# Kernel optimization log

Measured on AMD Instinct MI355X. Metric: run time of the kernel, lower is better.

Reference implementation:

```python
import jax, jax.numpy as jnp
import numpy as np

SEQ, MEM, B, H, NH, HD = 1024, 1024, 4, 1024, 16, 64
TOT = SEQ + MEM
RLEN = TOT
SCALE = 1.0 / np.sqrt(HD).astype(np.float32)
LN_EPS = 1e-5


def setup_inputs() -> dict:
    key = jax.random.key(0)
    ks = jax.random.split(key, 10)
    w = 0.02  # weight init scale
    # causal mask over memory+current segment: query i may attend keys j <= i + MEM
    i = jnp.arange(SEQ)[:, None]
    j = jnp.arange(TOT)[None, :]
    mask2d = j > (i + MEM)  # [SEQ, TOT] bool
    attn_mask = jnp.broadcast_to(mask2d[:, :, None], (SEQ, TOT, B))
    return {
        "x": jax.random.normal(ks[0], (SEQ, B, H), jnp.float32),
        "pos_embed": jax.random.normal(ks[1], (RLEN, H), jnp.float32),
        "r_w_bias": jax.random.normal(ks[2], (NH, HD), jnp.float32) * w,
        "r_r_bias": jax.random.normal(ks[3], (NH, HD), jnp.float32) * w,
        "attn_mask": attn_mask,
        "memory": jax.random.normal(ks[4], (MEM, B, H), jnp.float32),
        "W_qkv": jax.random.normal(ks[5], (3 * NH * HD, H), jnp.float32) * w,
        "W_r": jax.random.normal(ks[6], (NH * HD, H), jnp.float32) * w,
        "W_o": jax.random.normal(ks[7], (H, NH * HD), jnp.float32) * w,
        "ln_w": jnp.ones((H,), jnp.float32),
        "ln_b": jnp.zeros((H,), jnp.float32),
    }


def _layer_norm(x, w, b):
    mu = jnp.mean(x, axis=-1, keepdims=True)
    var = jnp.mean(jnp.square(x - mu), axis=-1, keepdims=True)
    return (x - mu) * jax.lax.rsqrt(var + LN_EPS) * w + b


def _rel_shift(x):
    # x: [i, j, b, n]; TXL rel-shift via pad-reshape-drop trick
    i, j, b, n = x.shape
    zp = jnp.zeros((i, 1, b, n), x.dtype)
    xp = jnp.concatenate([zp, x], axis=1)          # [i, j+1, b, n]
    xp = xp.reshape(j + 1, i, b, n)                # reinterpret row-major layout
    return xp[1:].reshape(i, j, b, n)


def reference(x, pos_embed, r_w_bias, r_r_bias, attn_mask, memory, W_qkv, W_r, W_o, ln_w, ln_b):
    full = jnp.concatenate([memory, x], axis=0)    # [TOT, B, H]
    w_heads = full @ W_qkv.T                       # [TOT, B, 3*NH*HD]
    q, k, v = jnp.split(w_heads, 3, axis=-1)
    q = q[-SEQ:].reshape(SEQ, B, NH, HD)
    k = k.reshape(TOT, B, NH, HD)
    v = v.reshape(TOT, B, NH, HD)
    r_k = (pos_embed @ W_r.T).reshape(RLEN, NH, HD)

    attn_ac = jnp.einsum('ibnd,jbnd->ijbn', q + r_w_bias, k)   # content score
    attn_bd = jnp.einsum('ibnd,jnd->ijbn', q + r_r_bias, r_k)  # position score
    attn_bd = _rel_shift(attn_bd)
    score = (attn_ac + attn_bd) * SCALE            # [SEQ, TOT, B, NH]
    score = jnp.where(attn_mask[:, :, :, None], -jnp.inf, score)
    prob = jax.nn.softmax(score, axis=1)           # softmax over key dim
    # dropout layers are identity in eval mode
    attn_vec = jnp.einsum('ijbn,jbnd->ibnd', prob, v).reshape(SEQ, B, NH * HD)
    attn_out = attn_vec @ W_o.T                    # [SEQ, B, H]
    return _layer_norm(x + attn_out, ln_w, ln_b)   # post-LN (pre_lnorm=False)
```

## Files before the change

### kernel.cpp

```cpp
#include <hip/hip_runtime.h>
#include <stdint.h>

typedef unsigned short u16;
typedef __bf16 bf16t;
typedef bf16t bf16x8 __attribute__((ext_vector_type(8)));
typedef float f32x4 __attribute__((ext_vector_type(4)));

#define DEV static __device__ __forceinline__

DEV u16 f2b(float f) {
  unsigned u = __float_as_uint(f);
  return (u16)((u + 0x7fffu + ((u >> 16) & 1u)) >> 16);
}
DEV u16 bcast(float f) {
  union { bf16t b; u16 u; } c;
  c.b = (bf16t)f;
  return c.u;
}
DEV float b2f(u16 h) { return __uint_as_float(((unsigned)h) << 16); }
DEV f32x4 fzero() { f32x4 v = {0.f, 0.f, 0.f, 0.f}; return v; }
DEV f32x4 mfma16(bf16x8 a, bf16x8 b, f32x4 c) {
  return __builtin_amdgcn_mfma_f32_16x16x32_bf16(a, b, c, 0, 0, 0);
}
DEV float exp2fast(float x) { return __builtin_amdgcn_exp2f(x); }

#define SEQ 1024
#define MEML 1024
#define BB 4
#define HH 1024
#define NHH 16
#define HDD 64
#define TOT 2048


__global__ __launch_bounds__(256) void k_pack(const float* __restrict__ mem,
                                              const float* __restrict__ x,
                                              u16* __restrict__ full) {
  size_t id4 = (size_t)blockIdx.x * 256 + threadIdx.x;
  size_t base = id4 * 4;
  int t = (int)(base >> 12);
  int rem = (int)(base & 4095);
  const float* src = (t < MEML) ? (mem + ((size_t)t << 12) + rem)
                                : (x + ((size_t)(t - MEML) << 12) + rem);
  float4 v = *(const float4*)src;
  ushort4 o;
  o.x = f2b(v.x); o.y = f2b(v.y); o.z = f2b(v.z); o.w = f2b(v.w);
  *(ushort4*)(full + base) = o;
}

__global__ __launch_bounds__(256) void k_cvt(const float* __restrict__ src,
                                             u16* __restrict__ dst, int n4) {
  int id = blockIdx.x * 256 + threadIdx.x;
  if (id >= n4) return;
  size_t base = (size_t)id * 4;
  float4 v = *(const float4*)(src + base);
  ushort4 o;
  o.x = f2b(v.x); o.y = f2b(v.y); o.z = f2b(v.z); o.w = f2b(v.w);
  *(ushort4*)(dst + base) = o;
}


template <int BM, int BN, int MF, int NF>
DEV void gemm_core(const u16* __restrict__ A, int lda, const u16* __restrict__ Bt,
                   int ldb, int K, f32x4 (&acc)[MF][NF]) {
  constexpr int WM = 16 * MF, WN = 16 * NF;
  constexpr int WAVES_M = BM / WM, WAVES_N = BN / WN;
  constexpr int THREADS = WAVES_M * WAVES_N * 64;
  constexpr int ITA = (BM * 4) / THREADS;
  constexpr int ITB = (BN * 4) / THREADS;
  __shared__ u16 As[BM * 40];
  __shared__ u16 Bs[BN * 40];
  const int tid = threadIdx.x, lane = tid & 63, wave = tid >> 6;
  const int wm = wave / WAVES_N, wn = wave % WAVES_N;
#pragma unroll
  for (int fm = 0; fm < MF; ++fm)
#pragma unroll
    for (int fn = 0; fn < NF; ++fn) acc[fm][fn] = fzero();

  for (int k0 = 0; k0 < K; k0 += 32) {
    __syncthreads();
#pragma unroll
    for (int it = 0; it < ITA; ++it) {
      int c = tid + it * THREADS;
      int r = c >> 2, kc = c & 3;
      *(uint4*)(As + r * 40 + kc * 8) =
          *(const uint4*)(A + (size_t)r * lda + k0 + kc * 8);
    }
#pragma unroll
    for (int it = 0; it < ITB; ++it) {
      int c = tid + it * THREADS;
      int r = c >> 2, kc = c & 3;
      *(uint4*)(Bs + r * 40 + kc * 8) =
          *(const uint4*)(Bt + (size_t)r * ldb + k0 + kc * 8);
    }
    __syncthreads();
    bf16x8 af[MF], bfr[NF];
#pragma unroll
    for (int fm = 0; fm < MF; ++fm)
      af[fm] = *(const bf16x8*)(As + (wm * WM + fm * 16 + (lane & 15)) * 40 +
                                ((lane >> 4) << 3));
#pragma unroll
    for (int fn = 0; fn < NF; ++fn)
      bfr[fn] = *(const bf16x8*)(Bs + (wn * WN + fn * 16 + (lane & 15)) * 40 +
                                 ((lane >> 4) << 3));
#pragma unroll
    for (int fm = 0; fm < MF; ++fm)
#pragma unroll
      for (int fn = 0; fn < NF; ++fn)
        acc[fm][fn] = mfma16(af[fm], bfr[fn], acc[fm][fn]);
  }
}

template <int BM, int BN, int MF, int NF, class F>
DEV void epi_apply(f32x4 (&acc)[MF][NF], F&& f) {
  constexpr int WAVES_N = BN / (16 * NF);
  const int lane = threadIdx.x & 63, wave = threadIdx.x >> 6;
  const int wm = wave / WAVES_N, wn = wave % WAVES_N;
#pragma unroll
  for (int fm = 0; fm < MF; ++fm)
#pragma unroll
    for (int fn = 0; fn < NF; ++fn)
#pragma unroll
      for (int q = 0; q < 4; ++q) {
        int rl = wm * (16 * MF) + fm * 16 + ((lane >> 4) << 2) + q;
        int cl = wn * (16 * NF) + fn * 16 + (lane & 15);
        f(rl, cl, acc[fm][fn][q]);
      }
}


__global__ __launch_bounds__(256) void k_gemm_qkv(
    const u16* __restrict__ full, const u16* __restrict__ wqkv,
    const float* __restrict__ rwb, const float* __restrict__ rrb,
    u16* __restrict__ qw, u16* __restrict__ qr, u16* __restrict__ kk,
    u16* __restrict__ vt) {
  f32x4 acc[4][4];
  const u16* A = full + (size_t)blockIdx.x * 128 * 1024;
  const u16* Bt = wqkv + (size_t)blockIdx.y * 128 * 1024;
  gemm_core<128, 128, 4, 4>(A, 1024, Bt, 1024, 1024, acc);
  const int row0 = blockIdx.x * 128, col0 = blockIdx.y * 128;
  epi_apply<128, 128, 4, 4>(acc, [&](int rl, int cl, float v) {
    int grow = row0 + rl, gcol = col0 + cl;
    int t = grow >> 2, bb = grow & 3;
    int which = gcol >> 10, hd = gcol & 1023;
    int n = hd >> 6, d = hd & 63;
    if (which == 0) {
      if (t >= MEML) {
        int i = t - MEML;
        size_t o = ((size_t)(bb * NHH + n) * SEQ + i) * HDD + d;
        qw[o] = f2b(v + rwb[hd]);
        qr[o] = f2b(v + rrb[hd]);
      }
    } else if (which == 1) {
      kk[((size_t)(bb * NHH + n) * TOT + t) * HDD + d] = f2b(v);
    } else {
      vt[((size_t)(bb * NHH + n) * HDD + d) * TOT + t] = f2b(v);
    }
  });
}

__global__ __launch_bounds__(256) void k_gemm_rk(const u16* __restrict__ pos,
                                                 const u16* __restrict__ wr,
                                                 u16* __restrict__ rk) {
  f32x4 acc[4][4];
  const u16* A = pos + (size_t)blockIdx.x * 128 * 1024;
  const u16* Bt = wr + (size_t)blockIdx.y * 128 * 1024;
  gemm_core<128, 128, 4, 4>(A, 1024, Bt, 1024, 1024, acc);
  const int row0 = blockIdx.x * 128, col0 = blockIdx.y * 128;
  epi_apply<128, 128, 4, 4>(acc, [&](int rl, int cl, float v) {
    int r = row0 + rl, o = col0 + cl;
    int n = o >> 6, d = o & 63;
    rk[((size_t)n * TOT + r) * HDD + d] = f2b(v);
  });
}

__global__ __launch_bounds__(256) void k_gemm_out(const u16* __restrict__ avec,
                                                  const u16* __restrict__ wo,
                                                  const float* __restrict__ x,
                                                  float* __restrict__ y) {
  f32x4 acc[4][4];
  const u16* A = avec + (size_t)blockIdx.x * 128 * 1024;
  const u16* Bt = wo + (size_t)blockIdx.y * 128 * 1024;
  gemm_core<128, 128, 4, 4>(A, 1024, Bt, 1024, 1024, acc);
  const int row0 = blockIdx.x * 128, col0 = blockIdx.y * 128;
  epi_apply<128, 128, 4, 4>(acc, [&](int rl, int cl, float v) {
    size_t o = (size_t)(row0 + rl) * HH + (col0 + cl);
    y[o] = v + x[o];
  });
}


__global__ __launch_bounds__(256, 2) void k_flash(
    const u16* __restrict__ qw, const u16* __restrict__ qr,
    const u16* __restrict__ kk, const u16* __restrict__ rk,
    const u16* __restrict__ vt, u16* __restrict__ avec) {
  __shared__ __align__(16) u16 Kb[2 * 4096];
  __shared__ __align__(16) u16 Vb[2 * 4096];
  __shared__ __align__(16) u16 BDp[64 * 136];
  __shared__ __align__(16) u16 Ps[4 * 1024];
  const int tid = threadIdx.x, lane = tid & 63, w = tid >> 6;
  const int l15 = lane & 15, g = lane >> 4;
  const int bid = blockIdx.x;
  const int work = (bid & 7) * 128 + (bid >> 3);
  const int ti = work & 15, pair = work >> 4;
  const int n = pair & 15, b = pair >> 4;
  const int i0 = ti * 64;
  const int bn = b * NHH + n;
  const u16* qwb = qw + ((size_t)bn * SEQ + i0) * HDD;
  const u16* qrb = qr + ((size_t)bn * SEQ + i0) * HDD;
  const u16* kbase = kk + (size_t)bn * TOT * HDD;
  const u16* rbase = rk + (size_t)n * TOT * HDD;
  const u16* vbase = vt + (size_t)bn * HDD * TOT;

  bf16x8 qwf[2], qrf[2];
#pragma unroll
  for (int ks = 0; ks < 2; ++ks) {
    int off = (w * 16 + l15) * HDD + ks * 32 + (g << 3);
    qwf[ks] = *(const bf16x8*)(qwb + off);
    qrf[ks] = *(const bf16x8*)(qrb + off);
  }

  const float NEGINF = -__builtin_inff();
  const float C2 = 0.125f * 1.44269504089f;
  f32x4 oacc[4];
#pragma unroll
  for (int db = 0; db < 4; ++db) oacc[db] = fzero();
  float mrow[4] = {NEGINF, NEGINF, NEGINF, NEGINF};
  float lrow[4] = {0.f, 0.f, 0.f, 0.f};

  const int m0 = 15 - ti;
  const int jtc = ti + 17;

  const int sr = (w << 4) + (lane >> 3);
  const int sc = (lane & 7) << 3;

  int bd_rd[16], bd_rs[16];
#pragma unroll
  for (int fn = 0; fn < 4; ++fn)
#pragma unroll
    for (int q = 0; q < 4; ++q) {
      int di = (w << 4) + (g << 2) + q;
      int dj = (fn << 4) + l15;
      int rl = (63 + dj - di) & 63;
      int s0 = ((1023 - i0 + dj - di) >> 6) & 1;
      int a0 = rl * 136 + s0 * 68 + di;
      int a1 = rl * 136 + (s0 ^ 1) * 68 + di;
      bd_rd[fn * 4 + q] = a0;
      bd_rs[fn * 4 + q] = a0 + a1;
    }
  int bd_wr[4], bd_ws[4];
  {
    int colw = (w << 4) + (g << 2);
    int sA = m0 & 1;
#pragma unroll
    for (int fn = 0; fn < 4; ++fn) {
      int wl = (fn << 4) + l15;
      int a0 = wl * 136 + sA * 68 + colw;
      int a1 = wl * 136 + (sA ^ 1) * 68 + colw;
      bd_wr[fn] = a0;
      bd_ws[fn] = a0 + a1;
    }
  }
  int ps_wr[16];
#pragma unroll
  for (int fn = 0; fn < 4; ++fn)
#pragma unroll
    for (int q = 0; q < 4; ++q) {
      int row = (g << 2) + q;
      ps_wr[fn * 4 + q] =
          (w << 10) + (row << 6) + ((((fn << 4) + l15)) ^ ((row & 7) << 3));
    }
  const int psr0 = (w << 10) + (l15 << 6) + ((g << 3) ^ ((l15 & 7) << 3));
  const int psr1 = psr0 ^ 32;
  int kr0 = (l15 << 6) + ((g << 3) ^ ((l15 & 7) << 3));
  int kr1 = kr0 ^ 32;
  int vr0 = kr0, vr1 = kr1;
  const int kwb = (sr << 6) + (sc ^ ((sr & 7) << 3));

  int koff = (64 + sr) * 64 + sc;
  int voff0 = sr * 2048 + 64 + sc;
  int voff1 = voff0 + 8 * 2048;
  int rvo[4];
#pragma unroll
  for (int fn = 0; fn < 4; ++fn)
    rvo[fn] = (((m0 + 2) << 6) + (fn << 4) + l15) * 64 + (g << 3);

  uint4 kg0, kg1, vg0, vg1;
  bf16x8 rfr[8];

  auto bd_comp_store = [&]() {
    f32x4 bd[4];
#pragma unroll
    for (int fn = 0; fn < 4; ++fn) bd[fn] = fzero();
#pragma unroll
    for (int ks = 0; ks < 2; ++ks)
#pragma unroll
      for (int fn = 0; fn < 4; ++fn)
        bd[fn] = mfma16(qrf[ks], rfr[ks * 4 + fn], bd[fn]);
#pragma unroll
    for (int fn = 0; fn < 4; ++fn) {
      ushort4 pk = {bcast(bd[fn][0] * C2), bcast(bd[fn][1] * C2),
                    bcast(bd[fn][2] * C2), bcast(bd[fn][3] * C2)};
      *(ushort4*)(BDp + bd_wr[fn]) = pk;
      bd_wr[fn] = bd_ws[fn] - bd_wr[fn];
    }
  };

  kg0 = *(const uint4*)(kbase + sr * 64 + sc);
  kg1 = *(const uint4*)(kbase + (sr + 8) * 64 + sc);
  vg0 = *(const uint4*)(vbase + sr * 2048 + sc);
  vg1 = *(const uint4*)(vbase + (sr + 8) * 2048 + sc);
#pragma unroll
  for (int fn = 0; fn < 4; ++fn) {
    int ro = ((m0 << 6) + (fn << 4) + l15) * 64 + (g << 3);
#pragma unroll
    for (int ks = 0; ks < 2; ++ks)
      rfr[ks * 4 + fn] = *(const bf16x8*)(rbase + ro + ks * 32);
  }
  bd_comp_store();
#pragma unroll
  for (int fn = 0; fn < 4; ++fn) {
    int ro = (((m0 + 1) << 6) + (fn << 4) + l15) * 64 + (g << 3);
#pragma unroll
    for (int ks = 0; ks < 2; ++ks)
      rfr[ks * 4 + fn] = *(const bf16x8*)(rbase + ro + ks * 32);
  }
  bd_comp_store();
  *(uint4*)(Kb + kwb) = kg0;
  *(uint4*)(Kb + kwb + 512) = kg1;
  *(uint4*)(Vb + kwb) = vg0;
  *(uint4*)(Vb + kwb + 512) = vg1;
  __syncthreads();
  int kw = kwb ^ 4096;

  for (int jt = 0; jt < jtc; ++jt) {
    const bool haveStage = (jt + 1 < jtc);
    const bool haveBD = (jt + 3 <= jtc);
    if (haveStage) {
      kg0 = *(const uint4*)(kbase + koff);
      kg1 = *(const uint4*)(kbase + koff + 512);
      vg0 = *(const uint4*)(vbase + voff0);
      vg1 = *(const uint4*)(vbase + voff1);
    }
    if (haveBD) {
#pragma unroll
      for (int fn = 0; fn < 4; ++fn)
#pragma unroll
        for (int ks = 0; ks < 2; ++ks)
          rfr[ks * 4 + fn] = *(const bf16x8*)(rbase + rvo[fn] + ks * 32);
    }

    f32x4 ac[4];
#pragma unroll
    for (int fn = 0; fn < 4; ++fn) ac[fn] = fzero();
#pragma unroll
    for (int fn = 0; fn < 4; ++fn) {
      bf16x8 kf = *(const bf16x8*)(Kb + kr0 + fn * 1024);
      ac[fn] = mfma16(qwf[0], kf, ac[fn]);
    }
#pragma unroll
    for (int fn = 0; fn < 4; ++fn) {
      bf16x8 kf = *(const bf16x8*)(Kb + kr1 + fn * 1024);
      ac[fn] = mfma16(qwf[1], kf, ac[fn]);
    }

    const bool last = (jt == jtc - 1);
    float pmax[4] = {NEGINF, NEGINF, NEGINF, NEGINF};
#pragma unroll
    for (int fn = 0; fn < 4; ++fn)
#pragma unroll
      for (int q = 0; q < 4; ++q) {
        float bdv = b2f(BDp[bd_rd[fn * 4 + q]]);
        float sv = __builtin_fmaf(ac[fn][q], C2, bdv);
        if (last) {
          int di = (g << 2) + q;
          int dj = (fn << 4) + l15 - (w << 4);
          if (dj > di) sv = NEGINF;
        }
        ac[fn][q] = sv;
        pmax[q] = fmaxf(pmax[q], sv);
      }
#pragma unroll
    for (int q = 0; q < 4; ++q) {
#pragma unroll
      for (int off = 1; off < 16; off <<= 1)
        pmax[q] = fmaxf(pmax[q], __shfl_xor(pmax[q], off, 64));
    }
    int need = (pmax[0] > mrow[0] + 8.f) | (pmax[1] > mrow[1] + 8.f) |
               (pmax[2] > mrow[2] + 8.f) | (pmax[3] > mrow[3] + 8.f);
    if (__any(need)) {
#pragma unroll
      for (int q = 0; q < 4; ++q) {
        float mn = fmaxf(mrow[q], pmax[q]);
        float sc2 = exp2fast(mrow[q] - mn);
        mrow[q] = mn;
        lrow[q] *= sc2;
#pragma unroll
        for (int db = 0; db < 4; ++db) oacc[db][q] *= sc2;
      }
    }
#pragma unroll
    for (int fn = 0; fn < 4; ++fn)
#pragma unroll
      for (int q = 0; q < 4; ++q) {
        float p = exp2fast(ac[fn][q] - mrow[q]);
        lrow[q] += p;
        Ps[ps_wr[fn * 4 + q]] = bcast(p);
      }
    {
      bf16x8 pa0 = *(const bf16x8*)(Ps + psr0);
      bf16x8 pa1 = *(const bf16x8*)(Ps + psr1);
#pragma unroll
      for (int db = 0; db < 4; ++db) {
        bf16x8 vf = *(const bf16x8*)(Vb + vr0 + db * 1024);
        oacc[db] = mfma16(pa0, vf, oacc[db]);
      }
#pragma unroll
      for (int db = 0; db < 4; ++db) {
        bf16x8 vf = *(const bf16x8*)(Vb + vr1 + db * 1024);
        oacc[db] = mfma16(pa1, vf, oacc[db]);
      }
    }
    if (haveBD) bd_comp_store();
    if (haveStage) {
      *(uint4*)(Kb + kw) = kg0;
      *(uint4*)(Kb + kw + 512) = kg1;
      *(uint4*)(Vb + kw) = vg0;
      *(uint4*)(Vb + kw + 512) = vg1;
    }
    __syncthreads();
#pragma unroll
    for (int e = 0; e < 16; ++e) bd_rd[e] = bd_rs[e] - bd_rd[e];
    kr0 ^= 4096; kr1 ^= 4096; vr0 ^= 4096; vr1 ^= 4096; kw ^= 4096;
    koff += 4096; voff0 += 64; voff1 += 64;
#pragma unroll
    for (int fn = 0; fn < 4; ++fn) rvo[fn] += 4096;
  }

#pragma unroll
  for (int q = 0; q < 4; ++q) {
#pragma unroll
    for (int off = 1; off < 16; off <<= 1)
      lrow[q] += __shfl_xor(lrow[q], off, 64);
    lrow[q] = 1.f / lrow[q];
  }
#pragma unroll
  for (int db = 0; db < 4; ++db)
#pragma unroll
    for (int q = 0; q < 4; ++q) {
      int i = i0 + (w << 4) + (g << 2) + q;
      avec[((size_t)i * BB + b) * HH + n * HDD + db * 16 + l15] =
          bcast(oacc[db][q] * lrow[q]);
    }
}


__global__ __launch_bounds__(256) void k_ln(const float* __restrict__ y,
                                            const float* __restrict__ lw,
                                            const float* __restrict__ lb,
                                            float* __restrict__ out) {
  const int row = blockIdx.x, tid = threadIdx.x;
  const float4 v = *(const float4*)(y + (size_t)row * HH + tid * 4);
  float s = v.x + v.y + v.z + v.w;
  float ss = v.x * v.x + v.y * v.y + v.z * v.z + v.w * v.w;
#pragma unroll
  for (int off = 1; off < 64; off <<= 1) {
    s += __shfl_xor(s, off, 64);
    ss += __shfl_xor(ss, off, 64);
  }
  __shared__ float red[8];
  const int w = tid >> 6, lane = tid & 63;
  if (lane == 0) { red[w] = s; red[4 + w] = ss; }
  __syncthreads();
  float tot = red[0] + red[1] + red[2] + red[3];
  float tss = red[4] + red[5] + red[6] + red[7];
  float mu = tot * (1.f / 1024.f);
  float var = tss * (1.f / 1024.f) - mu * mu;
  float rs = rsqrtf(var + 1e-5f);
  float4 wv = *(const float4*)(lw + tid * 4);
  float4 bv = *(const float4*)(lb + tid * 4);
  float4 o;
  o.x = (v.x - mu) * rs * wv.x + bv.x;
  o.y = (v.y - mu) * rs * wv.y + bv.y;
  o.z = (v.z - mu) * rs * wv.z + bv.z;
  o.w = (v.w - mu) * rs * wv.w + bv.w;
  *(float4*)(out + (size_t)row * HH + tid * 4) = o;
}


extern "C" void kernel_launch(void* const* d_in, const int* in_sizes, int n_in,
                              void* d_out, int out_size, void* d_ws,
                              size_t ws_size, hipStream_t stream) {
  const float* x = (const float*)d_in[0];
  const float* pos = (const float*)d_in[1];
  const float* rwb = (const float*)d_in[2];
  const float* rrb = (const float*)d_in[3];
  const float* mem = (const float*)d_in[5];
  const float* wqkv = (const float*)d_in[6];
  const float* wr = (const float*)d_in[7];
  const float* wo = (const float*)d_in[8];
  const float* lnw = (const float*)d_in[9];
  const float* lnb = (const float*)d_in[10];

  char* ws = (char*)d_ws;
  const size_t O_FULL = 0;
  const size_t O_WQKV = 16777216;
  const size_t O_WR = 23068672;
  const size_t O_WO = 25165824;
  const size_t O_POS = 27262976;
  const size_t O_QW = 31457280;
  const size_t O_QR = 39845888;
  const size_t O_K = 48234496;
  const size_t O_VT = 65011712;
  const size_t O_RK = 81788928;
  const size_t O_AVEC = 85983232;
  const size_t NEED = 94371840;

  if (ws_size < NEED) return;

  u16* full = (u16*)(ws + O_FULL);
  u16* wqkv_b = (u16*)(ws + O_WQKV);
  u16* wr_b = (u16*)(ws + O_WR);
  u16* wo_b = (u16*)(ws + O_WO);
  u16* pos_b = (u16*)(ws + O_POS);
  u16* qw = (u16*)(ws + O_QW);
  u16* qr = (u16*)(ws + O_QR);
  u16* kk = (u16*)(ws + O_K);
  u16* vt = (u16*)(ws + O_VT);
  u16* rk = (u16*)(ws + O_RK);
  u16* avec = (u16*)(ws + O_AVEC);
  float* y = (float*)(ws + O_FULL);

  k_pack<<<8192, 256, 0, stream>>>(mem, x, full);
  k_cvt<<<3072, 256, 0, stream>>>(wqkv, wqkv_b, 786432);
  k_cvt<<<1024, 256, 0, stream>>>(wr, wr_b, 262144);
  k_cvt<<<1024, 256, 0, stream>>>(wo, wo_b, 262144);
  k_cvt<<<2048, 256, 0, stream>>>(pos, pos_b, 524288);

  k_gemm_qkv<<<dim3(64, 24), 256, 0, stream>>>(full, wqkv_b, rwb, rrb, qw, qr,
                                               kk, vt);
  k_gemm_rk<<<dim3(16, 8), 256, 0, stream>>>(pos_b, wr_b, rk);

  k_flash<<<dim3(1024), 256, 0, stream>>>(qw, qr, kk, rk, vt, avec);

  k_gemm_out<<<dim3(32, 8), 256, 0, stream>>>(avec, wo_b, x, y);
  k_ln<<<4096, 256, 0, stream>>>(y, lnw, lnb, (float*)d_out);
}
```

Baseline: 340.6 us.

## Load GEMM tiles directly into LDS and schedule heavy attention tiles first

The shared GEMM core now copies A and B tiles from global memory straight into LDS with 16-byte global_load_lds, instead of staging them through registers. The LDS tiles become unpadded with a 32-element row stride so each wave's lane-ordered writes land contiguously. That unpadded layout can cause more LDS bank conflicts on the fragment reads. Separately, the flash attention kernel reverses the query-tile order so the tiles with the most unmasked keys are scheduled first, which should improve load balance across CUs.

```diff
diff --git a/kernel.cpp b/kernel.cpp
--- a/kernel.cpp
+++ b/kernel.cpp
@@ -23,6 +23,11 @@
   return __builtin_amdgcn_mfma_f32_16x16x32_bf16(a, b, c, 0, 0, 0);
 }
 DEV float exp2fast(float x) { return __builtin_amdgcn_exp2f(x); }
+DEV void gload16(const u16* g, u16* l) {
+  __builtin_amdgcn_global_load_lds(
+      (const __attribute__((address_space(1))) unsigned int*)g,
+      (__attribute__((address_space(3))) unsigned int*)l, 16, 0, 0);
+}
 
 #define SEQ 1024
 #define MEML 1024
@@ -60,49 +65,42 @@
 }
 
 
-template <int BM, int BN, int MF, int NF>
-DEV void gemm_core(const u16* __restrict__ A, int lda, const u16* __restrict__ Bt,
-                   int ldb, int K, f32x4 (&acc)[MF][NF]) {
-  constexpr int WM = 16 * MF, WN = 16 * NF;
-  constexpr int WAVES_M = BM / WM, WAVES_N = BN / WN;
-  constexpr int THREADS = WAVES_M * WAVES_N * 64;
-  constexpr int ITA = (BM * 4) / THREADS;
-  constexpr int ITB = (BN * 4) / THREADS;
-  __shared__ u16 As[BM * 40];
-  __shared__ u16 Bs[BN * 40];
+template <int MF, int NF>
+DEV void gemm_core2(const u16* __restrict__ A, int lda,
+                    const u16* __restrict__ Bt, int ldb, int K,
+                    f32x4 (&acc)[MF][NF]) {
+  __shared__ __align__(16) u16 As[128 * 32];
+  __shared__ __align__(16) u16 Bs[128 * 32];
   const int tid = threadIdx.x, lane = tid & 63, wave = tid >> 6;
-  const int wm = wave / WAVES_N, wn = wave % WAVES_N;
+  const int l15 = lane & 15, g = lane >> 4;
+  const int wm = wave >> 1, wn = wave & 1;
 #pragma unroll
   for (int fm = 0; fm < MF; ++fm)
 #pragma unroll
     for (int fn = 0; fn < NF; ++fn) acc[fm][fn] = fzero();
+
+  const int e8a = tid, e8b = 256 + tid;
+  const int ra0 = e8a >> 2, ca0 = (e8a & 3) << 3;
+  const int ra1 = e8b >> 2, ca1 = (e8b & 3) << 3;
+  u16* asd0 = As + (wave << 9);
+  u16* asd1 = As + 2048 + (wave << 9);
+  u16* bsd0 = Bs + (wave << 9);
+  u16* bsd1 = Bs + 2048 + (wave << 9);
 
   for (int k0 = 0; k0 < K; k0 += 32) {
     __syncthreads();
-#pragma unroll
-    for (int it = 0; it < ITA; ++it) {
-      int c = tid + it * THREADS;
-      int r = c >> 2, kc = c & 3;
-      *(uint4*)(As + r * 40 + kc * 8) =
-          *(const uint4*)(A + (size_t)r * lda + k0 + kc * 8);
-    }
-#pragma unroll
-    for (int it = 0; it < ITB; ++it) {
-      int c = tid + it * THREADS;
-      int r = c >> 2, kc = c & 3;
-      *(uint4*)(Bs + r * 40 + kc * 8) =
-          *(const uint4*)(Bt + (size_t)r * ldb + k0 + kc * 8);
-    }
+    gload16(A + (size_t)ra0 * lda + k0 + ca0, asd0);
+    gload16(A + (size_t)ra1 * lda + k0 + ca1, asd1);
+    gload16(Bt + (size_t)ra0 * ldb + k0 + ca0, bsd0);
+    gload16(Bt + (size_t)ra1 * ldb + k0 + ca1, bsd1);
     __syncthreads();
     bf16x8 af[MF], bfr[NF];
 #pragma unroll
     for (int fm = 0; fm < MF; ++fm)
-      af[fm] = *(const bf16x8*)(As + (wm * WM + fm * 16 + (lane & 15)) * 40 +
-                                ((lane >> 4) << 3));
+      af[fm] = *(const bf16x8*)(As + ((wm * 64 + fm * 16 + l15) << 5) + (g << 3));
 #pragma unroll
     for (int fn = 0; fn < NF; ++fn)
-      bfr[fn] = *(const bf16x8*)(Bs + (wn * WN + fn * 16 + (lane & 15)) * 40 +
-                                 ((lane >> 4) << 3));
+      bfr[fn] = *(const bf16x8*)(Bs + ((wn * 64 + fn * 16 + l15) << 5) + (g << 3));
 #pragma unroll
     for (int fm = 0; fm < MF; ++fm)
 #pragma unroll
@@ -137,7 +135,7 @@
   f32x4 acc[4][4];
   const u16* A = full + (size_t)blockIdx.x * 128 * 1024;
   const u16* Bt = wqkv + (size_t)blockIdx.y * 128 * 1024;
-  gemm_core<128, 128, 4, 4>(A, 1024, Bt, 1024, 1024, acc);
+  gemm_core2<4, 4>(A, 1024, Bt, 1024, 1024, acc);
   const int row0 = blockIdx.x * 128, col0 = blockIdx.y * 128;
   epi_apply<128, 128, 4, 4>(acc, [&](int rl, int cl, float v) {
     int grow = row0 + rl, gcol = col0 + cl;
@@ -165,7 +163,7 @@
   f32x4 acc[4][4];
   const u16* A = pos + (size_t)blockIdx.x * 128 * 1024;
   const u16* Bt = wr + (size_t)blockIdx.y * 128 * 1024;
-  gemm_core<128, 128, 4, 4>(A, 1024, Bt, 1024, 1024, acc);
+  gemm_core2<4, 4>(A, 1024, Bt, 1024, 1024, acc);
   const int row0 = blockIdx.x * 128, col0 = blockIdx.y * 128;
   epi_apply<128, 128, 4, 4>(acc, [&](int rl, int cl, float v) {
     int r = row0 + rl, o = col0 + cl;
@@ -181,7 +179,7 @@
   f32x4 acc[4][4];
   const u16* A = avec + (size_t)blockIdx.x * 128 * 1024;
   const u16* Bt = wo + (size_t)blockIdx.y * 128 * 1024;
-  gemm_core<128, 128, 4, 4>(A, 1024, Bt, 1024, 1024, acc);
+  gemm_core2<4, 4>(A, 1024, Bt, 1024, 1024, acc);
   const int row0 = blockIdx.x * 128, col0 = blockIdx.y * 128;
   epi_apply<128, 128, 4, 4>(acc, [&](int rl, int cl, float v) {
     size_t o = (size_t)(row0 + rl) * HH + (col0 + cl);
@@ -202,7 +200,8 @@
   const int l15 = lane & 15, g = lane >> 4;
   const int bid = blockIdx.x;
   const int work = (bid & 7) * 128 + (bid >> 3);
-  const int ti = work & 15, pair = work >> 4;
+  const int ti = 15 - (work & 15);
+  const int pair = work >> 4;
   const int n = pair & 15, b = pair >> 4;
   const int i0 = ti * 64;
   const int bn = b * NHH + n;
```

Result: faster. 300.5 us (-11.8%).
